# Kernel optimization log

Hardware: AMD Instinct MI355X
Metric: run time of the kernel (lower is better)

## Reference

```python
import jax, jax.numpy as jnp
import numpy as np

N, IN_DIM, OUT_DIM = 16384, 256, 128


def setup_inputs() -> dict:
    key = jax.random.key(0)
    k1, k2, k3, k4 = jax.random.split(key, 4)
    x = jax.random.normal(k1, (N, IN_DIM), dtype=jnp.float32)
    A_hat = jax.random.uniform(k2, (N, N), dtype=jnp.float32)
    # Linear params (torch nn.Linear default init scale ~ 1/sqrt(in_dim))
    bound = 1.0 / np.sqrt(IN_DIM)
    W = jax.random.uniform(k3, (OUT_DIM, IN_DIM), minval=-bound, maxval=bound, dtype=jnp.float32)
    b = jax.random.uniform(k4, (OUT_DIM,), minval=-bound, maxval=bound, dtype=jnp.float32)
    return {"x": x, "A_hat": A_hat, "W": W, "b": b}


def reference(x, A_hat, W, b):
    # h = x @ W^T + b : [N, out_dim]
    h = jnp.einsum("ni,oi->no", x, W) + b
    # aggregation: A_hat @ h : [N, out_dim]
    return A_hat @ h
```

## Files before the change

### kernel.cpp

```cpp
#include <hip/hip_runtime.h>


#define N_NODES 16384
#define IN_DIM  256
#define OUT_DIM 128

typedef short bf16x8 __attribute__((ext_vector_type(8)));
typedef float f32x4  __attribute__((ext_vector_type(4)));

__device__ __forceinline__ unsigned short f2bf(float f) {
    unsigned u = __float_as_uint(f);
    u += 0x7fffu + ((u >> 16) & 1u);
    return (unsigned short)(u >> 16);
}

__device__ __forceinline__ bf16x8 load_cvt8(const float* __restrict__ p) {
    f32x4 a = *reinterpret_cast<const f32x4*>(p);
    f32x4 c = *reinterpret_cast<const f32x4*>(p + 4);
    bf16x8 r;
#pragma unroll
    for (int i = 0; i < 4; ++i) {
        r[i]     = (short)f2bf(a[i]);
        r[i + 4] = (short)f2bf(c[i]);
    }
    return r;
}

__global__ __launch_bounds__(256) void gemm1_xw(
    const float* __restrict__ x, const float* __restrict__ W,
    const float* __restrict__ b, unsigned short* __restrict__ hT) {
    const int tid  = threadIdx.x;
    const int lane = tid & 63, wid = tid >> 6;
    const int l16  = lane & 15, quad = lane >> 4;
    const int n0   = blockIdx.x * 128;
    const int wm   = (wid >> 1) * 64;
    const int wn   = (wid & 1) * 64;

    f32x4 acc[4][4] = {};

    const float* aBase = W + (size_t)(wm + l16) * IN_DIM + quad * 8;
    const float* bBase = x + (size_t)(n0 + wn + l16) * IN_DIM + quad * 8;

#pragma unroll 2
    for (int k = 0; k < IN_DIM; k += 32) {
        bf16x8 af[4], bfr[4];
#pragma unroll
        for (int mf = 0; mf < 4; ++mf)
            af[mf] = load_cvt8(aBase + (size_t)mf * 16 * IN_DIM + k);
#pragma unroll
        for (int nf = 0; nf < 4; ++nf)
            bfr[nf] = load_cvt8(bBase + (size_t)nf * 16 * IN_DIM + k);
#pragma unroll
        for (int mf = 0; mf < 4; ++mf)
#pragma unroll
            for (int nf = 0; nf < 4; ++nf)
                acc[mf][nf] = __builtin_amdgcn_mfma_f32_16x16x32_bf16(
                    af[mf], bfr[nf], acc[mf][nf], 0, 0, 0);
    }

#pragma unroll
    for (int mf = 0; mf < 4; ++mf) {
#pragma unroll
        for (int i = 0; i < 4; ++i) {
            const int o    = wm + mf * 16 + quad * 4 + i;
            const float bo = b[o];
#pragma unroll
            for (int nf = 0; nf < 4; ++nf) {
                const int n = n0 + wn + nf * 16 + l16;
                hT[(size_t)o * N_NODES + n] = f2bf(acc[mf][nf][i] + bo);
            }
        }
    }
}

__global__ __launch_bounds__(256) void gemm2_ah(
    const float* __restrict__ A, const unsigned short* __restrict__ hT,
    float* __restrict__ out) {
    const int tid  = threadIdx.x;
    const int lane = tid & 63, wid = tid >> 6;
    const int l16  = lane & 15, quad = lane >> 4;
    const int m0   = blockIdx.x * 64;
    const int wm   = (wid >> 1) * 32;
    const int wn   = (wid & 1) * 64;

    f32x4 acc[2][4] = {};

    const float*          aBase = A  + (size_t)(m0 + wm + l16) * N_NODES + quad * 8;
    const unsigned short* bBase = hT + (size_t)(wn + l16) * N_NODES + quad * 8;

#pragma unroll 2
    for (int k = 0; k < N_NODES; k += 32) {
        bf16x8 af[2], bfr[4];
#pragma unroll
        for (int mf = 0; mf < 2; ++mf)
            af[mf] = load_cvt8(aBase + (size_t)mf * 16 * N_NODES + k);
#pragma unroll
        for (int nf = 0; nf < 4; ++nf)
            bfr[nf] = *reinterpret_cast<const bf16x8*>(
                bBase + (size_t)nf * 16 * N_NODES + k);
#pragma unroll
        for (int mf = 0; mf < 2; ++mf)
#pragma unroll
            for (int nf = 0; nf < 4; ++nf)
                acc[mf][nf] = __builtin_amdgcn_mfma_f32_16x16x32_bf16(
                    af[mf], bfr[nf], acc[mf][nf], 0, 0, 0);
    }

#pragma unroll
    for (int mf = 0; mf < 2; ++mf)
#pragma unroll
        for (int i = 0; i < 4; ++i) {
            const int row = m0 + wm + mf * 16 + quad * 4 + i;
#pragma unroll
            for (int nf = 0; nf < 4; ++nf) {
                const int col = wn + nf * 16 + l16;
                out[(size_t)row * OUT_DIM + col] = acc[mf][nf][i];
            }
        }
}

extern "C" void kernel_launch(void* const* d_in, const int* in_sizes, int n_in,
                              void* d_out, int out_size, void* d_ws, size_t ws_size,
                              hipStream_t stream) {
    const float* x     = (const float*)d_in[0];
    const float* A_hat = (const float*)d_in[1];
    const float* W     = (const float*)d_in[2];
    const float* b     = (const float*)d_in[3];
    float* out         = (float*)d_out;
    unsigned short* hT = (unsigned short*)d_ws;

    gemm1_xw<<<N_NODES / 128, 256, 0, stream>>>(x, W, b, hT);
    gemm2_ah<<<N_NODES / 64, 256, 0, stream>>>(A_hat, hT, out);
}
```

Baseline: 1.636 ms.

## Pre-swizzle h into MFMA fragment layout and shrink GEMM2 tiles with nontemporal A loads

GEMM1 now writes h in a fragment-tiled layout, so each lane in GEMM2 loads its B fragment as one contiguous 8-element chunk and a wavefront reads 1KB contiguous blocks. GEMM2 drops to a 32-row block tile (one M fragment per wave) to double the grid size, and it streams A_hat with nontemporal loads and writes the output with nontemporal stores. The aim is more parallelism on the memory-bound A_hat stream and less cache pollution. In exchange h is re-read twice as often per A row, and GEMM1 also uses smaller tiles.

```diff
diff --git a/kernel.cpp b/kernel.cpp
--- a/kernel.cpp
+++ b/kernel.cpp
@@ -14,9 +14,7 @@
     return (unsigned short)(u >> 16);
 }
 
-__device__ __forceinline__ bf16x8 load_cvt8(const float* __restrict__ p) {
-    f32x4 a = *reinterpret_cast<const f32x4*>(p);
-    f32x4 c = *reinterpret_cast<const f32x4*>(p + 4);
+__device__ __forceinline__ bf16x8 cvt8(f32x4 a, f32x4 c) {
     bf16x8 r;
 #pragma unroll
     for (int i = 0; i < 4; ++i) {
@@ -26,34 +24,45 @@
     return r;
 }
 
+__device__ __forceinline__ bf16x8 load_cvt8(const float* __restrict__ p) {
+    return cvt8(*reinterpret_cast<const f32x4*>(p),
+                *reinterpret_cast<const f32x4*>(p + 4));
+}
+
+__device__ __forceinline__ bf16x8 load_cvt8_nt(const float* __restrict__ p) {
+    f32x4 a = __builtin_nontemporal_load(reinterpret_cast<const f32x4*>(p));
+    f32x4 c = __builtin_nontemporal_load(reinterpret_cast<const f32x4*>(p) + 1);
+    return cvt8(a, c);
+}
+
 __global__ __launch_bounds__(256) void gemm1_xw(
     const float* __restrict__ x, const float* __restrict__ W,
     const float* __restrict__ b, unsigned short* __restrict__ hT) {
     const int tid  = threadIdx.x;
     const int lane = tid & 63, wid = tid >> 6;
     const int l16  = lane & 15, quad = lane >> 4;
-    const int n0   = blockIdx.x * 128;
+    const int n0   = blockIdx.x * 64;
     const int wm   = (wid >> 1) * 64;
-    const int wn   = (wid & 1) * 64;
+    const int wn   = (wid & 1) * 32;
 
-    f32x4 acc[4][4] = {};
+    f32x4 acc[4][2] = {};
 
     const float* aBase = W + (size_t)(wm + l16) * IN_DIM + quad * 8;
     const float* bBase = x + (size_t)(n0 + wn + l16) * IN_DIM + quad * 8;
 
 #pragma unroll 2
     for (int k = 0; k < IN_DIM; k += 32) {
-        bf16x8 af[4], bfr[4];
+        bf16x8 af[4], bfr[2];
 #pragma unroll
         for (int mf = 0; mf < 4; ++mf)
             af[mf] = load_cvt8(aBase + (size_t)mf * 16 * IN_DIM + k);
 #pragma unroll
-        for (int nf = 0; nf < 4; ++nf)
+        for (int nf = 0; nf < 2; ++nf)
             bfr[nf] = load_cvt8(bBase + (size_t)nf * 16 * IN_DIM + k);
 #pragma unroll
         for (int mf = 0; mf < 4; ++mf)
 #pragma unroll
-            for (int nf = 0; nf < 4; ++nf)
+            for (int nf = 0; nf < 2; ++nf)
                 acc[mf][nf] = __builtin_amdgcn_mfma_f32_16x16x32_bf16(
                     af[mf], bfr[nf], acc[mf][nf], 0, 0, 0);
     }
@@ -65,9 +74,11 @@
             const int o    = wm + mf * 16 + quad * 4 + i;
             const float bo = b[o];
 #pragma unroll
-            for (int nf = 0; nf < 4; ++nf) {
+            for (int nf = 0; nf < 2; ++nf) {
                 const int n = n0 + wn + nf * 16 + l16;
-                hT[(size_t)o * N_NODES + n] = f2bf(acc[mf][nf][i] + bo);
+                const size_t idx = (size_t)((n >> 5) * 8 + (o >> 4)) * 512
+                                 + ((n >> 3) & 3) * 128 + (o & 15) * 8 + (n & 7);
+                hT[idx] = f2bf(acc[mf][nf][i] + bo);
             }
         }
     }
@@ -79,44 +90,40 @@
     const int tid  = threadIdx.x;
     const int lane = tid & 63, wid = tid >> 6;
     const int l16  = lane & 15, quad = lane >> 4;
-    const int m0   = blockIdx.x * 64;
-    const int wm   = (wid >> 1) * 32;
+    const int m0   = blockIdx.x * 32;
+    const int wm   = (wid >> 1) * 16;
     const int wn   = (wid & 1) * 64;
+    const int otile = wn >> 4;
 
-    f32x4 acc[2][4] = {};
+    f32x4 acc[4] = {};
 
     const float*          aBase = A  + (size_t)(m0 + wm + l16) * N_NODES + quad * 8;
-    const unsigned short* bBase = hT + (size_t)(wn + l16) * N_NODES + quad * 8;
+    const unsigned short* bBase = hT + (size_t)lane * 8 + (size_t)otile * 512;
 
-#pragma unroll 2
+#pragma unroll 4
     for (int k = 0; k < N_NODES; k += 32) {
-        bf16x8 af[2], bfr[4];
-#pragma unroll
-        for (int mf = 0; mf < 2; ++mf)
-            af[mf] = load_cvt8(aBase + (size_t)mf * 16 * N_NODES + k);
+        bf16x8 af = load_cvt8_nt(aBase + k);
+        const unsigned short* bk = bBase + (size_t)(k >> 5) * 4096;
+        bf16x8 bfr[4];
 #pragma unroll
         for (int nf = 0; nf < 4; ++nf)
-            bfr[nf] = *reinterpret_cast<const bf16x8*>(
-                bBase + (size_t)nf * 16 * N_NODES + k);
+            bfr[nf] = *reinterpret_cast<const bf16x8*>(bk + nf * 512);
 #pragma unroll
-        for (int mf = 0; mf < 2; ++mf)
-#pragma unroll
-            for (int nf = 0; nf < 4; ++nf)
-                acc[mf][nf] = __builtin_amdgcn_mfma_f32_16x16x32_bf16(
-                    af[mf], bfr[nf], acc[mf][nf], 0, 0, 0);
+        for (int nf = 0; nf < 4; ++nf)
+            acc[nf] = __builtin_amdgcn_mfma_f32_16x16x32_bf16(
+                af, bfr[nf], acc[nf], 0, 0, 0);
     }
 
 #pragma unroll
-    for (int mf = 0; mf < 2; ++mf)
+    for (int i = 0; i < 4; ++i) {
+        const int row = m0 + wm + quad * 4 + i;
 #pragma unroll
-        for (int i = 0; i < 4; ++i) {
-            const int row = m0 + wm + mf * 16 + quad * 4 + i;
-#pragma unroll
-            for (int nf = 0; nf < 4; ++nf) {
-                const int col = wn + nf * 16 + l16;
-                out[(size_t)row * OUT_DIM + col] = acc[mf][nf][i];
-            }
+        for (int nf = 0; nf < 4; ++nf) {
+            const int col = wn + nf * 16 + l16;
+            __builtin_nontemporal_store(acc[nf][i],
+                                        out + (size_t)row * OUT_DIM + col);
         }
+    }
 }
 
 extern "C" void kernel_launch(void* const* d_in, const int* in_sizes, int n_in,
@@ -129,6 +136,6 @@
     float* out         = (float*)d_out;
     unsigned short* hT = (unsigned short*)d_ws;
 
-    gemm1_xw<<<N_NODES / 128, 256, 0, stream>>>(x, W, b, hT);
-    gemm2_ah<<<N_NODES / 64, 256, 0, stream>>>(A_hat, hT, out);
+    gemm1_xw<<<N_NODES / 64, 256, 0, stream>>>(x, W, b, hT);
+    gemm2_ah<<<N_NODES / 32, 256, 0, stream>>>(A_hat, hT, out);
 }
```

New measurement: 1.746 ms. 6.8% more time.
